# Kernel optimization log

Measured on AMD Instinct MI355X. Metric: run time of the kernel, lower is better.

The kernel has to match this reference:

```python
import jax, jax.numpy as jnp
import numpy as np

_INV_SQRT2 = np.float32(0.7071067811865476)


def _dwt_last(u):
    """Single-level Haar DWT along the last axis (pywt 'haar' convention).
    cA[i] = (u[2i]+u[2i+1])/sqrt(2), cD[i] = (u[2i]-u[2i+1])/sqrt(2)."""
    e = u[..., 0::2]
    o = u[..., 1::2]
    return (e + o) * _INV_SQRT2, (e - o) * _INV_SQRT2


def _dwt2(x):
    """Single-level 2D Haar DWT over the last two axes, matching pywt.dwt2.
    Returns (cA, cH, cV, cD) = ('aa', 'da', 'ad', 'dd') where the first
    letter is the filter applied along axis -2 and the second along axis -1."""
    a1, d1 = _dwt_last(x)                      # filter along axis -1
    a1t, d1t = a1.swapaxes(-1, -2), d1.swapaxes(-1, -2)
    aa, da = _dwt_last(a1t)                    # filter along axis -2
    ad, dd = _dwt_last(d1t)
    return (aa.swapaxes(-1, -2), da.swapaxes(-1, -2),
            ad.swapaxes(-1, -2), dd.swapaxes(-1, -2))


def setup_inputs() -> dict:
    key = jax.random.key(0)
    B, C, H, W = 32, 3, 512, 512
    x = jax.random.normal(key, (B, C, H, W), dtype=jnp.float32)
    return {"x": x}


def reference(x):
    # pywt.wavedec2(x, 'haar', level=2) -> [cA2, (cH2,cV2,cD2), (cH1,cV1,cD1)]
    a1, h1, v1, d1 = _dwt2(x)    # level 1: [B,C,H/2,W/2]
    a2, h2, v2, d2 = _dwt2(a1)   # level 2: [B,C,H/4,W/4]
    return (a2, h2, v2, d2, h1, v1, d1)
```

## Files before the change

### kernel.cpp

```cpp
#include <hip/hip_runtime.h>


#define KINV 0.7071067811865476f

__global__ __launch_bounds__(256) void haar2_fused_kernel(
    const float* __restrict__ x, float* __restrict__ out, int nimg)
{
    const int tid = blockIdx.x * blockDim.x + threadIdx.x;
    const int total = nimg * 128 * 128;
    if (tid >= total) return;

    const int c2  = tid & 127;
    const int r2  = (tid >> 7) & 127;
    const int img = tid >> 14;

    const float* xin = x + (size_t)img * (512 * 512);
    const int row0 = r2 * 4;
    const int col0 = c2 * 4;

    float p[4][4];
    #pragma unroll
    for (int k = 0; k < 4; ++k) {
        float4 v = *reinterpret_cast<const float4*>(xin + (size_t)(row0 + k) * 512 + col0);
        p[k][0] = v.x; p[k][1] = v.y; p[k][2] = v.z; p[k][3] = v.w;
    }

    float aa[2][2], da[2][2], ad[2][2], dd[2][2];
    #pragma unroll
    for (int i = 0; i < 2; ++i) {
        #pragma unroll
        for (int j = 0; j < 2; ++j) {
            const float p00 = p[2*i    ][2*j], p01 = p[2*i    ][2*j+1];
            const float p10 = p[2*i + 1][2*j], p11 = p[2*i + 1][2*j+1];
            const float sA = (p00 + p01) * KINV;
            const float sB = (p10 + p11) * KINV;
            const float dA = (p00 - p01) * KINV;
            const float dB = (p10 - p11) * KINV;
            aa[i][j] = (sA + sB) * KINV;
            da[i][j] = (sA - sB) * KINV;
            ad[i][j] = (dA + dB) * KINV;
            dd[i][j] = (dA - dB) * KINV;
        }
    }

    const size_t n2 = (size_t)nimg * 128 * 128;
    const size_t n1 = (size_t)nimg * 256 * 256;
    float* a2o = out;
    float* h2o = out + n2;
    float* v2o = out + 2 * n2;
    float* d2o = out + 3 * n2;
    float* h1o = out + 4 * n2;
    float* v1o = h1o + n1;
    float* d1o = h1o + 2 * n1;

    const size_t img1 = (size_t)img * 256 * 256;
    #pragma unroll
    for (int i = 0; i < 2; ++i) {
        const size_t off = img1 + (size_t)(2 * r2 + i) * 256 + 2 * c2;
        *reinterpret_cast<float2*>(h1o + off) = make_float2(da[i][0], da[i][1]);
        *reinterpret_cast<float2*>(v1o + off) = make_float2(ad[i][0], ad[i][1]);
        *reinterpret_cast<float2*>(d1o + off) = make_float2(dd[i][0], dd[i][1]);
    }

    const float s0 = (aa[0][0] + aa[0][1]) * KINV;
    const float d0 = (aa[0][0] - aa[0][1]) * KINV;
    const float s1 = (aa[1][0] + aa[1][1]) * KINV;
    const float d1 = (aa[1][0] - aa[1][1]) * KINV;
    const size_t off2 = (size_t)img * 128 * 128 + (size_t)r2 * 128 + c2;
    a2o[off2] = (s0 + s1) * KINV;
    h2o[off2] = (s0 - s1) * KINV;
    v2o[off2] = (d0 + d1) * KINV;
    d2o[off2] = (d0 - d1) * KINV;
}

extern "C" void kernel_launch(void* const* d_in, const int* in_sizes, int n_in,
                              void* d_out, int out_size, void* d_ws, size_t ws_size,
                              hipStream_t stream) {
    const float* x = (const float*)d_in[0];
    float* out = (float*)d_out;
    const int nimg = in_sizes[0] / (512 * 512);
    const int total = nimg * 128 * 128;
    const int block = 256;
    const int grid = (total + block - 1) / block;
    haar2_fused_kernel<<<grid, block, 0, stream>>>(x, out, nimg);
}
```

Baseline: 175.5 us.

## Loop each thread over images with double-buffered register prefetch

Each thread now handles eight images spaced twelve apart instead of one, and loads the next image's 4x4 patch into registers while it computes and stores the current one. The grid shrinks to a fixed 12 images' worth of threads, which cuts block launch overhead and keeps more loads in flight per thread. It hardcodes 96 images (12 x 8) with no bounds check, so any other input size would be processed wrongly.

```diff
diff --git a/kernel.cpp b/kernel.cpp
--- a/kernel.cpp
+++ b/kernel.cpp
@@ -3,45 +3,22 @@
 
 #define KINV 0.7071067811865476f
 
+typedef float v4f __attribute__((ext_vector_type(4)));
+typedef float v2f __attribute__((ext_vector_type(2)));
+
+#define IMG_STRIDE 12
+#define NITER 8
+
 __global__ __launch_bounds__(256) void haar2_fused_kernel(
     const float* __restrict__ x, float* __restrict__ out, int nimg)
 {
     const int tid = blockIdx.x * blockDim.x + threadIdx.x;
-    const int total = nimg * 128 * 128;
-    if (tid >= total) return;
+    const int c2   = tid & 127;
+    const int r2   = (tid >> 7) & 127;
+    const int img0 = tid >> 14;
 
-    const int c2  = tid & 127;
-    const int r2  = (tid >> 7) & 127;
-    const int img = tid >> 14;
-
-    const float* xin = x + (size_t)img * (512 * 512);
     const int row0 = r2 * 4;
     const int col0 = c2 * 4;
-
-    float p[4][4];
-    #pragma unroll
-    for (int k = 0; k < 4; ++k) {
-        float4 v = *reinterpret_cast<const float4*>(xin + (size_t)(row0 + k) * 512 + col0);
-        p[k][0] = v.x; p[k][1] = v.y; p[k][2] = v.z; p[k][3] = v.w;
-    }
-
-    float aa[2][2], da[2][2], ad[2][2], dd[2][2];
-    #pragma unroll
-    for (int i = 0; i < 2; ++i) {
-        #pragma unroll
-        for (int j = 0; j < 2; ++j) {
-            const float p00 = p[2*i    ][2*j], p01 = p[2*i    ][2*j+1];
-            const float p10 = p[2*i + 1][2*j], p11 = p[2*i + 1][2*j+1];
-            const float sA = (p00 + p01) * KINV;
-            const float sB = (p10 + p11) * KINV;
-            const float dA = (p00 - p01) * KINV;
-            const float dB = (p10 - p11) * KINV;
-            aa[i][j] = (sA + sB) * KINV;
-            da[i][j] = (sA - sB) * KINV;
-            ad[i][j] = (dA + dB) * KINV;
-            dd[i][j] = (dA - dB) * KINV;
-        }
-    }
 
     const size_t n2 = (size_t)nimg * 128 * 128;
     const size_t n1 = (size_t)nimg * 256 * 256;
@@ -53,24 +30,69 @@
     float* v1o = h1o + n1;
     float* d1o = h1o + 2 * n1;
 
-    const size_t img1 = (size_t)img * 256 * 256;
+    const size_t in_base = (size_t)img0 * (512 * 512) + (size_t)row0 * 512 + col0;
+    const size_t in_step = (size_t)IMG_STRIDE * 512 * 512;
+
+    v4f buf[2][4];
     #pragma unroll
-    for (int i = 0; i < 2; ++i) {
-        const size_t off = img1 + (size_t)(2 * r2 + i) * 256 + 2 * c2;
-        *reinterpret_cast<float2*>(h1o + off) = make_float2(da[i][0], da[i][1]);
-        *reinterpret_cast<float2*>(v1o + off) = make_float2(ad[i][0], ad[i][1]);
-        *reinterpret_cast<float2*>(d1o + off) = make_float2(dd[i][0], dd[i][1]);
+    for (int k = 0; k < 4; ++k)
+        buf[0][k] = *reinterpret_cast<const v4f*>(x + in_base + (size_t)k * 512);
+
+    #pragma unroll
+    for (int it = 0; it < NITER; ++it) {
+        const int cur = it & 1;
+        if (it + 1 < NITER) {
+            const size_t nb = in_base + (size_t)(it + 1) * in_step;
+            #pragma unroll
+            for (int k = 0; k < 4; ++k)
+                buf[cur ^ 1][k] = *reinterpret_cast<const v4f*>(x + nb + (size_t)k * 512);
+        }
+
+        const int img = img0 + it * IMG_STRIDE;
+        float p[4][4];
+        #pragma unroll
+        for (int k = 0; k < 4; ++k) {
+            p[k][0] = buf[cur][k].x; p[k][1] = buf[cur][k].y;
+            p[k][2] = buf[cur][k].z; p[k][3] = buf[cur][k].w;
+        }
+
+        float aa[2][2], da[2][2], ad[2][2], dd[2][2];
+        #pragma unroll
+        for (int i = 0; i < 2; ++i) {
+            #pragma unroll
+            for (int j = 0; j < 2; ++j) {
+                const float p00 = p[2*i    ][2*j], p01 = p[2*i    ][2*j+1];
+                const float p10 = p[2*i + 1][2*j], p11 = p[2*i + 1][2*j+1];
+                const float sA = (p00 + p01) * KINV;
+                const float sB = (p10 + p11) * KINV;
+                const float dA = (p00 - p01) * KINV;
+                const float dB = (p10 - p11) * KINV;
+                aa[i][j] = (sA + sB) * KINV;
+                da[i][j] = (sA - sB) * KINV;
+                ad[i][j] = (dA + dB) * KINV;
+                dd[i][j] = (dA - dB) * KINV;
+            }
+        }
+
+        const size_t img1 = (size_t)img * 256 * 256;
+        #pragma unroll
+        for (int i = 0; i < 2; ++i) {
+            const size_t off = img1 + (size_t)(2 * r2 + i) * 256 + 2 * c2;
+            *reinterpret_cast<v2f*>(h1o + off) = (v2f){da[i][0], da[i][1]};
+            *reinterpret_cast<v2f*>(v1o + off) = (v2f){ad[i][0], ad[i][1]};
+            *reinterpret_cast<v2f*>(d1o + off) = (v2f){dd[i][0], dd[i][1]};
+        }
+
+        const float s0 = (aa[0][0] + aa[0][1]) * KINV;
+        const float d0 = (aa[0][0] - aa[0][1]) * KINV;
+        const float s1 = (aa[1][0] + aa[1][1]) * KINV;
+        const float d1 = (aa[1][0] - aa[1][1]) * KINV;
+        const size_t off2 = (size_t)img * 128 * 128 + (size_t)r2 * 128 + c2;
+        a2o[off2] = (s0 + s1) * KINV;
+        h2o[off2] = (s0 - s1) * KINV;
+        v2o[off2] = (d0 + d1) * KINV;
+        d2o[off2] = (d0 - d1) * KINV;
     }
-
-    const float s0 = (aa[0][0] + aa[0][1]) * KINV;
-    const float d0 = (aa[0][0] - aa[0][1]) * KINV;
-    const float s1 = (aa[1][0] + aa[1][1]) * KINV;
-    const float d1 = (aa[1][0] - aa[1][1]) * KINV;
-    const size_t off2 = (size_t)img * 128 * 128 + (size_t)r2 * 128 + c2;
-    a2o[off2] = (s0 + s1) * KINV;
-    h2o[off2] = (s0 - s1) * KINV;
-    v2o[off2] = (d0 + d1) * KINV;
-    d2o[off2] = (d0 - d1) * KINV;
 }
 
 extern "C" void kernel_launch(void* const* d_in, const int* in_sizes, int n_in,
@@ -79,8 +101,8 @@
     const float* x = (const float*)d_in[0];
     float* out = (float*)d_out;
     const int nimg = in_sizes[0] / (512 * 512);
-    const int total = nimg * 128 * 128;
+    const int total_threads = IMG_STRIDE * 128 * 128;
     const int block = 256;
-    const int grid = (total + block - 1) / block;
+    const int grid = total_threads / block;
     haar2_fused_kernel<<<grid, block, 0, stream>>>(x, out, nimg);
 }
```

Result: no change. 174.6 us (-0.5%).
